# Kernel tuning notes

Hardware: AMD Instinct MI355X
Metric: run time of the kernel (lower is better)

## Reference

```python
import jax, jax.numpy as jnp
import numpy as np
import math

D_MODEL = 1024
N_HEADS = 16
D_HEAD = D_MODEL // N_HEADS
B, L = 4, 2048


def setup_inputs() -> dict:
    key = jax.random.key(0)
    ks = jax.random.split(key, 9)
    s = 1.0 / math.sqrt(D_MODEL)
    x = jax.random.normal(ks[0], (B, L, D_MODEL), dtype=jnp.float32)
    # causal mask, broadcastable over batch and heads
    attn_mask = jnp.tril(jnp.ones((L, L), dtype=jnp.int32))[None, None, :, :]
    Wq = jax.random.uniform(ks[1], (D_MODEL, D_MODEL), jnp.float32, -s, s)
    bq = jax.random.uniform(ks[2], (D_MODEL,), jnp.float32, -s, s)
    Wk = jax.random.uniform(ks[3], (D_MODEL, D_MODEL), jnp.float32, -s, s)
    bk = jax.random.uniform(ks[4], (D_MODEL,), jnp.float32, -s, s)
    Wv = jax.random.uniform(ks[5], (D_MODEL, D_MODEL), jnp.float32, -s, s)
    bv = jax.random.uniform(ks[6], (D_MODEL,), jnp.float32, -s, s)
    Wo = jax.random.uniform(ks[7], (D_MODEL, D_MODEL), jnp.float32, -s, s)
    bo = jax.random.uniform(ks[8], (D_MODEL,), jnp.float32, -s, s)
    return {"x": x, "attn_mask": attn_mask, "Wq": Wq, "bq": bq, "Wk": Wk,
            "bk": bk, "Wv": Wv, "bv": bv, "Wo": Wo, "bo": bo}


def reference(x, attn_mask, Wq, bq, Wk, bk, Wv, bv, Wo, bo):
    Bn, Ln, Dn = x.shape
    scale = 1.0 / math.sqrt(D_HEAD)

    def split_heads(t):  # [B,L,D] -> [B,H,L,dh]
        return t.reshape(Bn, Ln, N_HEADS, D_HEAD).transpose(0, 2, 1, 3)

    q = split_heads(x @ Wq + bq)
    k = split_heads(x @ Wk + bk)
    v = split_heads(x @ Wv + bv)
    scores = jnp.einsum('bhqd,bhkd->bhqk', q, k) * scale
    scores = jnp.where(attn_mask == 0, jnp.float32(-jnp.inf), scores)
    attn = jax.nn.softmax(scores, axis=-1)  # dropout p=0.0 -> identity
    ctx = jnp.einsum('bhqk,bhkd->bhqd', attn, v)
    ctx = ctx.transpose(0, 2, 1, 3).reshape(Bn, Ln, Dn)
    return ctx @ Wo + bo
```

## Files before the change

### kernel.cpp

```cpp
#include <hip/hip_runtime.h>


typedef unsigned short u16;
typedef __attribute__((ext_vector_type(8))) short short8;
typedef __attribute__((ext_vector_type(4))) float floatx4;
typedef __attribute__((ext_vector_type(2))) unsigned int uint2v;

#define NEG_BIG (-1e30f)
#define SCL_LOG2E 0.1803368801111244f

__device__ __forceinline__ u16 f2bf(float f) {
  unsigned int u = __builtin_bit_cast(unsigned int, f);
  u += 0x7fffu + ((u >> 16) & 1u);
  return (u16)(u >> 16);
}

__device__ __forceinline__ short8 cvt8(const float* __restrict__ p) {
  const floatx4 a = *(const floatx4*)p;
  const floatx4 b = *(const floatx4*)(p + 4);
  short8 r;
  r[0] = (short)f2bf(a[0]); r[1] = (short)f2bf(a[1]);
  r[2] = (short)f2bf(a[2]); r[3] = (short)f2bf(a[3]);
  r[4] = (short)f2bf(b[0]); r[5] = (short)f2bf(b[1]);
  r[6] = (short)f2bf(b[2]); r[7] = (short)f2bf(b[3]);
  return r;
}

__device__ __forceinline__ void gll16(const u16* g, u16* l) {
  __builtin_amdgcn_global_load_lds((const __attribute__((address_space(1))) void*)g,
                                   (__attribute__((address_space(3))) void*)l,
                                   16, 0, 0);
}

__global__ void cvt_x(const float* __restrict__ x, u16* __restrict__ xb) {
  const int i = blockIdx.x * 256 + threadIdx.x;
  *(short8*)(xb + (size_t)i * 8) = cvt8(x + (size_t)i * 8);
}

__global__ void transpose4(const float* __restrict__ s0, const float* __restrict__ s1,
                           const float* __restrict__ s2, const float* __restrict__ s3,
                           u16* __restrict__ d0, u16* __restrict__ d1,
                           u16* __restrict__ d2, u16* __restrict__ d3) {
  __shared__ u16 tile[64][72];
  const float* src; u16* dst;
  switch (blockIdx.z) {
    case 0: src = s0; dst = d0; break;
    case 1: src = s1; dst = d1; break;
    case 2: src = s2; dst = d2; break;
    default: src = s3; dst = d3; break;
  }
  const int t = threadIdx.x;
  const int c = t & 63, rg = t >> 6;
  const int x0 = blockIdx.x * 64, y0 = blockIdx.y * 64;
#pragma unroll
  for (int i = 0; i < 16; ++i) {
    const int row = rg * 16 + i;
    tile[row][c] = f2bf(src[(size_t)(y0 + row) * 1024 + x0 + c]);
  }
  __syncthreads();
#pragma unroll
  for (int i = 0; i < 16; ++i) {
    const int row = rg * 16 + i;
    dst[(size_t)(x0 + row) * 1024 + y0 + c] = tile[c][row];
  }
}

__global__ void transpose_v(const u16* __restrict__ Vb, u16* __restrict__ Vt) {
  __shared__ u16 tile[64][66];
  const int bh = blockIdx.y;
  const int l0 = blockIdx.x * 64;
  const size_t base = (size_t)bh * (2048 * 64);
  const int t = threadIdx.x;
#pragma unroll
  for (int c = t; c < 512; c += 256) {
    const int row = c >> 3, cc = c & 7;
    *(short8*)&tile[row][cc * 8] =
        *(const short8*)(Vb + base + (size_t)(l0 + row) * 64 + cc * 8);
  }
  __syncthreads();
  const int c2 = t & 63, rg = t >> 6;
#pragma unroll
  for (int i = 0; i < 16; ++i) {
    const int dr = rg * 16 + i;
    Vt[base + (size_t)dr * 2048 + l0 + c2] = tile[c2][dr];
  }
}

__global__ __launch_bounds__(256, 2) void gemm_qkv(
    const u16* __restrict__ A, const u16* __restrict__ Bt,
    const float* __restrict__ bq, const float* __restrict__ bk,
    const float* __restrict__ bv,
    u16* __restrict__ Qb, u16* __restrict__ Kb, u16* __restrict__ Vb) {
  const int K = 1024;
  __shared__ __align__(16) u16 As[128 * 32];
  __shared__ __align__(16) u16 Bs[128 * 32];
  const int t = threadIdx.x;
  const int w = t >> 6, l = t & 63;
  const int quad = l >> 4, l16 = l & 15;
  const int m0 = blockIdx.y * 128, n0 = blockIdx.x * 128;
  const int wr = w >> 1, wc = w & 1;

  floatx4 acc[4][4] = {};

  for (int k0 = 0; k0 < K; k0 += 32) {
    __syncthreads();
#pragma unroll
    for (int p = 0; p < 2; ++p) {
      const int c0 = (p * 4 + w) * 64;
      const int c = c0 + l;
      const int row = c >> 2;
      const int koff = (c & 3) * 8;
      gll16(A + (size_t)(m0 + row) * K + k0 + koff, &As[c0 * 8]);
      gll16(Bt + (size_t)(n0 + row) * K + k0 + koff, &Bs[c0 * 8]);
    }
    __syncthreads();

    short8 af[4], bf[4];
#pragma unroll
    for (int i = 0; i < 4; ++i)
      af[i] = *(const short8*)&As[(wr * 64 + i * 16 + l16) * 32 + quad * 8];
#pragma unroll
    for (int j = 0; j < 4; ++j)
      bf[j] = *(const short8*)&Bs[(wc * 64 + j * 16 + l16) * 32 + quad * 8];
#pragma unroll
    for (int i = 0; i < 4; ++i)
#pragma unroll
      for (int j = 0; j < 4; ++j)
        acc[i][j] = __builtin_amdgcn_mfma_f32_16x16x32_bf16(af[i], bf[j], acc[i][j], 0, 0, 0);
  }

  const int seg = n0 >> 10;
  const float* bias = (seg == 0) ? bq : (seg == 1) ? bk : bv;
  u16* dst = (seg == 0) ? Qb : (seg == 1) ? Kb : Vb;
#pragma unroll
  for (int j = 0; j < 4; ++j) {
    const int nn = (n0 & 1023) + wc * 64 + j * 16 + l16;
    const float bvs = bias[nn];
    const int h = nn >> 6, dh = nn & 63;
#pragma unroll
    for (int i = 0; i < 4; ++i) {
      const int rb = m0 + wr * 64 + i * 16 + quad * 4;
#pragma unroll
      for (int r = 0; r < 4; ++r) {
        const int m = rb + r;
        const int b = m >> 11, ll = m & 2047;
        dst[((size_t)(b * 16 + h) * 2048 + ll) * 64 + dh] = f2bf(acc[i][j][r] + bvs);
      }
    }
  }
}

__global__ __launch_bounds__(256, 2) void gemm_out(
    const u16* __restrict__ A, const u16* __restrict__ Bt,
    const float* __restrict__ bias, float* __restrict__ C, int M, int N, int K) {
  __shared__ __align__(16) u16 As[128 * 32];
  __shared__ __align__(16) u16 Bs[128 * 32];
  const int t = threadIdx.x;
  const int w = t >> 6, l = t & 63;
  const int quad = l >> 4, l16 = l & 15;
  const int m0 = blockIdx.y * 128, n0 = blockIdx.x * 128;
  const int wr = w >> 1, wc = w & 1;

  floatx4 acc[4][4] = {};

  for (int k0 = 0; k0 < K; k0 += 32) {
    __syncthreads();
#pragma unroll
    for (int p = 0; p < 2; ++p) {
      const int c0 = (p * 4 + w) * 64;
      const int c = c0 + l;
      const int row = c >> 2;
      const int koff = (c & 3) * 8;
      gll16(A + (size_t)(m0 + row) * K + k0 + koff, &As[c0 * 8]);
      gll16(Bt + (size_t)(n0 + row) * K + k0 + koff, &Bs[c0 * 8]);
    }
    __syncthreads();

    short8 af[4], bf[4];
#pragma unroll
    for (int i = 0; i < 4; ++i)
      af[i] = *(const short8*)&As[(wr * 64 + i * 16 + l16) * 32 + quad * 8];
#pragma unroll
    for (int j = 0; j < 4; ++j)
      bf[j] = *(const short8*)&Bs[(wc * 64 + j * 16 + l16) * 32 + quad * 8];
#pragma unroll
    for (int i = 0; i < 4; ++i)
#pragma unroll
      for (int j = 0; j < 4; ++j)
        acc[i][j] = __builtin_amdgcn_mfma_f32_16x16x32_bf16(af[i], bf[j], acc[i][j], 0, 0, 0);
  }

#pragma unroll
  for (int j = 0; j < 4; ++j) {
    const int n = n0 + wc * 64 + j * 16 + l16;
    const float bvs = bias[n];
#pragma unroll
    for (int i = 0; i < 4; ++i) {
      const int rb = m0 + wr * 64 + i * 16 + quad * 4;
#pragma unroll
      for (int r = 0; r < 4; ++r)
        C[(size_t)(rb + r) * N + n] = acc[i][j][r] + bvs;
    }
  }
}

__global__ __launch_bounds__(256, 4) void attn_kernel(
    const u16* __restrict__ Q, const u16* __restrict__ K,
    const u16* __restrict__ Vt, u16* __restrict__ ctx) {
  __shared__ __align__(16) u16 Ks[2][64 * 64];
  __shared__ __align__(16) u16 Vs[2][64 * 64];
  __shared__ __align__(16) u16 Ps[4 * 16 * 64];

  const int t = threadIdx.x;
  const int w = t >> 6, l = t & 63;
  const int quad = l >> 4, l16 = l & 15;
  const int bh = blockIdx.y;
  const size_t base = (size_t)bh * (2048 * 64);
  u16* Pw = &Ps[w * 16 * 64];
  unsigned int* Pw32 = (unsigned int*)Pw;
  const int b = bh >> 4, h = bh & 15;

  const int pc0 = w * 64 + l, pc1 = (4 + w) * 64 + l;
  const int sr0 = pc0 >> 3, sc0 = (pc0 & 7) ^ (sr0 & 7);
  const int sr1 = pc1 >> 3, sc1 = (pc1 & 7) ^ (sr1 & 7);
  const int swz = (l16 & 7);

  auto run_seg = [&](int q0, int nkt) {
    short8 aq[2];
#pragma unroll
    for (int ks = 0; ks < 2; ++ks)
      aq[ks] = *(const short8*)(Q + base + (size_t)(q0 + w * 16 + l16) * 64 + ks * 32 + quad * 8);

    gll16(K + base + (size_t)sr0 * 64 + sc0 * 8, &Ks[0][(w * 64) * 8]);
    gll16(K + base + (size_t)sr1 * 64 + sc1 * 8, &Ks[0][((4 + w) * 64) * 8]);
    gll16(Vt + base + (size_t)sr0 * 2048 + sc0 * 8, &Vs[0][(w * 64) * 8]);
    gll16(Vt + base + (size_t)sr1 * 2048 + sc1 * 8, &Vs[0][((4 + w) * 64) * 8]);

    floatx4 o[4] = {};
    float mrun = NEG_BIG, lsum = 0.f;

    auto body = [&](int kt, bool diag) {
      const int cur = kt & 1, nxt = cur ^ 1;
      __syncthreads();
      if (!diag) {
        const int kn = (kt + 1) * 64;
        gll16(K + base + (size_t)(kn + sr0) * 64 + sc0 * 8, &Ks[nxt][(w * 64) * 8]);
        gll16(K + base + (size_t)(kn + sr1) * 64 + sc1 * 8, &Ks[nxt][((4 + w) * 64) * 8]);
        gll16(Vt + base + (size_t)sr0 * 2048 + kn + sc0 * 8, &Vs[nxt][(w * 64) * 8]);
        gll16(Vt + base + (size_t)sr1 * 2048 + kn + sc1 * 8, &Vs[nxt][((4 + w) * 64) * 8]);
      }

      floatx4 s[4] = {};
#pragma unroll
      for (int ks = 0; ks < 2; ++ks)
#pragma unroll
        for (int tn = 0; tn < 4; ++tn) {
          const short8 bk = *(const short8*)&Ks[cur][(tn * 16 + l16) * 64 + (((ks * 4 + quad) ^ swz) << 3)];
          s[tn] = __builtin_amdgcn_mfma_f32_16x16x32_bf16(bk, aq[ks], s[tn], 0, 0, 0);
        }

      float mx = NEG_BIG;
#pragma unroll
      for (int tn = 0; tn < 4; ++tn)
#pragma unroll
        for (int r = 0; r < 4; ++r) {
          float v = s[tn][r] * SCL_LOG2E;
          if (diag && (tn * 16 + quad * 4 + r > w * 16 + l16)) v = NEG_BIG;
          s[tn][r] = v;
          mx = fmaxf(mx, v);
        }
      mx = fmaxf(mx, __shfl_xor(mx, 16));
      mx = fmaxf(mx, __shfl_xor(mx, 32));

      const float mnew = fmaxf(mrun, mx);
      const float alpha = exp2f(mrun - mnew);
      mrun = mnew;
      float rs = 0.f;
#pragma unroll
      for (int tn = 0; tn < 4; ++tn)
#pragma unroll
        for (int r = 0; r < 4; ++r) {
          const float p = exp2f(s[tn][r] - mnew);
          s[tn][r] = p;
          rs += p;
        }
      rs += __shfl_xor(rs, 16);
      rs += __shfl_xor(rs, 32);
      lsum = lsum * alpha + rs;
#pragma unroll
      for (int td = 0; td < 4; ++td)
#pragma unroll
        for (int r = 0; r < 4; ++r) o[td][r] *= alpha;

#pragma unroll
      for (int tn = 0; tn < 4; ++tn) {
        unsigned int p0, p1;
        asm("v_cvt_pk_bf16_f32 %0, %1, %2"
            : "=v"(p0) : "v"(s[tn][0]), "v"(s[tn][1]));
        asm("v_cvt_pk_bf16_f32 %0, %1, %2"
            : "=v"(p1) : "v"(s[tn][2]), "v"(s[tn][3]));
        const int cc = (2 * tn + (quad >> 1)) ^ swz;
        uint2v pr; pr.x = p0; pr.y = p1;
        *(uint2v*)&Pw32[l16 * 32 + cc * 4 + 2 * (quad & 1)] = pr;
      }
      __asm__ volatile("s_waitcnt lgkmcnt(0)" ::: "memory");
      __builtin_amdgcn_wave_barrier();

      short8 ap[2];
#pragma unroll
      for (int ks = 0; ks < 2; ++ks)
        ap[ks] = *(const short8*)&Pw[l16 * 64 + (((ks * 4 + quad) ^ swz) << 3)];

#pragma unroll
      for (int ks = 0; ks < 2; ++ks)
#pragma unroll
        for (int td = 0; td < 4; ++td) {
          const short8 bv = *(const short8*)&Vs[cur][(td * 16 + l16) * 64 + (((ks * 4 + quad) ^ swz) << 3)];
          o[td] = __builtin_amdgcn_mfma_f32_16x16x32_bf16(bv, ap[ks], o[td], 0, 0, 0);
        }
    };

    for (int kt = 0; kt < nkt - 1; ++kt) body(kt, false);
    body(nkt - 1, true);

    const float inv = 1.f / lsum;
    const int gq = q0 + w * 16 + l16;
    u16* crow = ctx + ((size_t)(b * 2048 + gq)) * 1024 + h * 64;
#pragma unroll
    for (int td = 0; td < 4; ++td) {
      unsigned int lo, hi;
      asm("v_cvt_pk_bf16_f32 %0, %1, %2"
          : "=v"(lo) : "v"(o[td][0] * inv), "v"(o[td][1] * inv));
      asm("v_cvt_pk_bf16_f32 %0, %1, %2"
          : "=v"(hi) : "v"(o[td][2] * inv), "v"(o[td][3] * inv));
      uint2v pk;
      pk.x = lo; pk.y = hi;
      *(uint2v*)(crow + td * 16 + quad * 4) = pk;
    }
  };

  const int bx = blockIdx.x;
  run_seg((31 - bx) * 64, 32 - bx);
  __syncthreads();
  run_seg(bx * 64, bx + 1);
}

extern "C" void kernel_launch(void* const* d_in, const int* in_sizes, int n_in,
                              void* d_out, int out_size, void* d_ws, size_t ws_size,
                              hipStream_t stream) {
  const float* x  = (const float*)d_in[0];
  const float* Wq = (const float*)d_in[2];
  const float* bq = (const float*)d_in[3];
  const float* Wk = (const float*)d_in[4];
  const float* bk = (const float*)d_in[5];
  const float* Wv = (const float*)d_in[6];
  const float* bv = (const float*)d_in[7];
  const float* Wo = (const float*)d_in[8];
  const float* bo = (const float*)d_in[9];

  u16* ws = (u16*)d_ws;
  const size_t WSZ = 1u << 20;
  const size_t TSZ = 8u << 20;
  u16* WqT = ws;
  u16* WkT = ws + WSZ;
  u16* WvT = ws + 2 * WSZ;
  u16* WoT = ws + 3 * WSZ;
  u16* xb  = ws + 4 * WSZ;
  u16* Qb  = xb + TSZ;
  u16* Kb  = Qb + TSZ;
  u16* Vb  = Kb + TSZ;
  u16* Vtb = xb;
  u16* Ctx = Vb;

  const dim3 tb(256);
  cvt_x<<<dim3(4096), tb, 0, stream>>>(x, xb);
  transpose4<<<dim3(16, 16, 4), tb, 0, stream>>>(Wq, Wk, Wv, Wo, WqT, WkT, WvT, WoT);
  gemm_qkv<<<dim3(24, 64), tb, 0, stream>>>(xb, WqT, bq, bk, bv, Qb, Kb, Vb);
  transpose_v<<<dim3(32, 64), tb, 0, stream>>>(Vb, Vtb);
  attn_kernel<<<dim3(16, 64), tb, 0, stream>>>(Qb, Kb, Vtb, Ctx);
  gemm_out<<<dim3(8, 64), tb, 0, stream>>>(Ctx, WoT, bo, (float*)d_out, 8192, 1024, 1024);
}
```

Baseline: 299.5 us.

## Rewrite attention with 32x32 MFMA, register-resident K/V and XCD-aware block mapping

The attention kernel now drops LDS staging for K/V and P. Each wave loads K and V fragments straight from global memory into registers, uses 32x32x16 MFMAs on 32-key tiles, and reshuffles P through cross-lane shuffles instead of LDS. The softmax scale is folded into Q in the QKV GEMM epilogue, and output rescaling is skipped when no row max rises. Blocks are remapped so each XCD handles a fixed set of heads, with per-wave causal work pairing and a halved grid. This removes LDS traffic and block barriers, but adds redundant global loads across waves and makes performance depend on L2 and cache locality.

```diff
diff --git a/kernel.cpp b/kernel.cpp
--- a/kernel.cpp
+++ b/kernel.cpp
@@ -4,7 +4,9 @@
 typedef unsigned short u16;
 typedef __attribute__((ext_vector_type(8))) short short8;
 typedef __attribute__((ext_vector_type(4))) float floatx4;
+typedef __attribute__((ext_vector_type(16))) float floatx16;
 typedef __attribute__((ext_vector_type(2))) unsigned int uint2v;
+typedef __attribute__((ext_vector_type(4))) unsigned int uint4v;
 
 #define NEG_BIG (-1e30f)
 #define SCL_LOG2E 0.1803368801111244f
@@ -132,6 +134,7 @@
   const int seg = n0 >> 10;
   const float* bias = (seg == 0) ? bq : (seg == 1) ? bk : bv;
   u16* dst = (seg == 0) ? Qb : (seg == 1) ? Kb : Vb;
+  const float scl = (seg == 0) ? SCL_LOG2E : 1.0f;
 #pragma unroll
   for (int j = 0; j < 4; ++j) {
     const int nn = (n0 & 1023) + wc * 64 + j * 16 + l16;
@@ -144,7 +147,7 @@
       for (int r = 0; r < 4; ++r) {
         const int m = rb + r;
         const int b = m >> 11, ll = m & 2047;
-        dst[((size_t)(b * 16 + h) * 2048 + ll) * 64 + dh] = f2bf(acc[i][j][r] + bvs);
+        dst[((size_t)(b * 16 + h) * 2048 + ll) * 64 + dh] = f2bf((acc[i][j][r] + bvs) * scl);
       }
     }
   }
@@ -204,145 +207,138 @@
   }
 }
 
-__global__ __launch_bounds__(256, 4) void attn_kernel(
+__global__ __launch_bounds__(256, 2) void attn_kernel(
     const u16* __restrict__ Q, const u16* __restrict__ K,
     const u16* __restrict__ Vt, u16* __restrict__ ctx) {
-  __shared__ __align__(16) u16 Ks[2][64 * 64];
-  __shared__ __align__(16) u16 Vs[2][64 * 64];
-  __shared__ __align__(16) u16 Ps[4 * 16 * 64];
-
   const int t = threadIdx.x;
   const int w = t >> 6, l = t & 63;
-  const int quad = l >> 4, l16 = l & 15;
-  const int bh = blockIdx.y;
+  const int l32 = l & 31, hi = l >> 5;
+
+  const int lin = blockIdx.y * 8 + blockIdx.x;
+  const int xcd = lin & 7, m = lin >> 3;
+  const int bh = xcd * 8 + (m & 7);
+  const int pairp = m >> 3;
   const size_t base = (size_t)bh * (2048 * 64);
-  u16* Pw = &Ps[w * 16 * 64];
-  unsigned int* Pw32 = (unsigned int*)Pw;
   const int b = bh >> 4, h = bh & 15;
 
-  const int pc0 = w * 64 + l, pc1 = (4 + w) * 64 + l;
-  const int sr0 = pc0 >> 3, sc0 = (pc0 & 7) ^ (sr0 & 7);
-  const int sr1 = pc1 >> 3, sc1 = (pc1 & 7) ^ (sr1 & 7);
-  const int swz = (l16 & 7);
-
-  auto run_seg = [&](int q0, int nkt) {
-    short8 aq[2];
-#pragma unroll
-    for (int ks = 0; ks < 2; ++ks)
-      aq[ks] = *(const short8*)(Q + base + (size_t)(q0 + w * 16 + l16) * 64 + ks * 32 + quad * 8);
-
-    gll16(K + base + (size_t)sr0 * 64 + sc0 * 8, &Ks[0][(w * 64) * 8]);
-    gll16(K + base + (size_t)sr1 * 64 + sc1 * 8, &Ks[0][((4 + w) * 64) * 8]);
-    gll16(Vt + base + (size_t)sr0 * 2048 + sc0 * 8, &Vs[0][(w * 64) * 8]);
-    gll16(Vt + base + (size_t)sr1 * 2048 + sc1 * 8, &Vs[0][((4 + w) * 64) * 8]);
-
-    floatx4 o[4] = {};
+  auto seg = [&](int qblk, int qw) {
+    const int qsub = qblk * 128 + qw * 32;
+    const int nkt = qblk * 4 + qw + 1;
+    const int qg = qsub + l32;
+
+    short8 qf[4];
+#pragma unroll
+    for (int ks = 0; ks < 4; ++ks)
+      qf[ks] = *(const short8*)(Q + base + (size_t)qg * 64 + ks * 16 + hi * 8);
+    short8 kf[4];
+#pragma unroll
+    for (int ks = 0; ks < 4; ++ks)
+      kf[ks] = *(const short8*)(K + base + (size_t)l32 * 64 + ks * 16 + hi * 8);
+
+    floatx16 o0 = {}, o1 = {};
     float mrun = NEG_BIG, lsum = 0.f;
 
     auto body = [&](int kt, bool diag) {
-      const int cur = kt & 1, nxt = cur ^ 1;
-      __syncthreads();
+      short8 vf[4];
+#pragma unroll
+      for (int dw = 0; dw < 2; ++dw)
+#pragma unroll
+        for (int k2 = 0; k2 < 2; ++k2)
+          vf[dw * 2 + k2] = *(const short8*)(Vt + base + (size_t)(dw * 32 + l32) * 2048 +
+                                             kt * 32 + k2 * 16 + hi * 8);
+
+      floatx16 sA = {};
+#pragma unroll
+      for (int ks = 0; ks < 4; ++ks)
+        sA = __builtin_amdgcn_mfma_f32_32x32x16_bf16(kf[ks], qf[ks], sA, 0, 0, 0);
+
       if (!diag) {
-        const int kn = (kt + 1) * 64;
-        gll16(K + base + (size_t)(kn + sr0) * 64 + sc0 * 8, &Ks[nxt][(w * 64) * 8]);
-        gll16(K + base + (size_t)(kn + sr1) * 64 + sc1 * 8, &Ks[nxt][((4 + w) * 64) * 8]);
-        gll16(Vt + base + (size_t)sr0 * 2048 + kn + sc0 * 8, &Vs[nxt][(w * 64) * 8]);
-        gll16(Vt + base + (size_t)sr1 * 2048 + kn + sc1 * 8, &Vs[nxt][((4 + w) * 64) * 8]);
-      }
-
-      floatx4 s[4] = {};
-#pragma unroll
-      for (int ks = 0; ks < 2; ++ks)
-#pragma unroll
-        for (int tn = 0; tn < 4; ++tn) {
-          const short8 bk = *(const short8*)&Ks[cur][(tn * 16 + l16) * 64 + (((ks * 4 + quad) ^ swz) << 3)];
-          s[tn] = __builtin_amdgcn_mfma_f32_16x16x32_bf16(bk, aq[ks], s[tn], 0, 0, 0);
-        }
+#pragma unroll
+        for (int ks = 0; ks < 4; ++ks)
+          kf[ks] = *(const short8*)(K + base + (size_t)((kt + 1) * 32 + l32) * 64 +
+                                    ks * 16 + hi * 8);
+      }
 
       float mx = NEG_BIG;
-#pragma unroll
-      for (int tn = 0; tn < 4; ++tn)
-#pragma unroll
-        for (int r = 0; r < 4; ++r) {
-          float v = s[tn][r] * SCL_LOG2E;
-          if (diag && (tn * 16 + quad * 4 + r > w * 16 + l16)) v = NEG_BIG;
-          s[tn][r] = v;
+      if (diag) {
+#pragma unroll
+        for (int r = 0; r < 16; ++r) {
+          const int krow = (r & 3) + 8 * (r >> 2) + 4 * hi;
+          float v = sA[r];
+          if (krow > l32) v = NEG_BIG;
+          sA[r] = v;
           mx = fmaxf(mx, v);
         }
-      mx = fmaxf(mx, __shfl_xor(mx, 16));
+      } else {
+#pragma unroll
+        for (int r = 0; r < 16; ++r) mx = fmaxf(mx, sA[r]);
+      }
       mx = fmaxf(mx, __shfl_xor(mx, 32));
 
-      const float mnew = fmaxf(mrun, mx);
-      const float alpha = exp2f(mrun - mnew);
-      mrun = mnew;
+      if (__any(mx > mrun)) {
+        const float mnew = fmaxf(mrun, mx);
+        const float al = exp2f(mrun - mnew);
+        mrun = mnew;
+        lsum *= al;
+#pragma unroll
+        for (int r = 0; r < 16; ++r) { o0[r] *= al; o1[r] *= al; }
+      }
+
       float rs = 0.f;
 #pragma unroll
-      for (int tn = 0; tn < 4; ++tn)
-#pragma unroll
-        for (int r = 0; r < 4; ++r) {
-          const float p = exp2f(s[tn][r] - mnew);
-          s[tn][r] = p;
-          rs += p;
-        }
-      rs += __shfl_xor(rs, 16);
+      for (int r = 0; r < 16; ++r) {
+        const float p = exp2f(sA[r] - mrun);
+        sA[r] = p;
+        rs += p;
+      }
       rs += __shfl_xor(rs, 32);
-      lsum = lsum * alpha + rs;
-#pragma unroll
-      for (int td = 0; td < 4; ++td)
-#pragma unroll
-        for (int r = 0; r < 4; ++r) o[td][r] *= alpha;
-
-#pragma unroll
-      for (int tn = 0; tn < 4; ++tn) {
-        unsigned int p0, p1;
+      lsum += rs;
+
+      unsigned int wv[8], xv[8];
+#pragma unroll
+      for (int i = 0; i < 8; ++i)
         asm("v_cvt_pk_bf16_f32 %0, %1, %2"
-            : "=v"(p0) : "v"(s[tn][0]), "v"(s[tn][1]));
-        asm("v_cvt_pk_bf16_f32 %0, %1, %2"
-            : "=v"(p1) : "v"(s[tn][2]), "v"(s[tn][3]));
-        const int cc = (2 * tn + (quad >> 1)) ^ swz;
-        uint2v pr; pr.x = p0; pr.y = p1;
-        *(uint2v*)&Pw32[l16 * 32 + cc * 4 + 2 * (quad & 1)] = pr;
-      }
-      __asm__ volatile("s_waitcnt lgkmcnt(0)" ::: "memory");
-      __builtin_amdgcn_wave_barrier();
-
-      short8 ap[2];
-#pragma unroll
-      for (int ks = 0; ks < 2; ++ks)
-        ap[ks] = *(const short8*)&Pw[l16 * 64 + (((ks * 4 + quad) ^ swz) << 3)];
-
-#pragma unroll
-      for (int ks = 0; ks < 2; ++ks)
-#pragma unroll
-        for (int td = 0; td < 4; ++td) {
-          const short8 bv = *(const short8*)&Vs[cur][(td * 16 + l16) * 64 + (((ks * 4 + quad) ^ swz) << 3)];
-          o[td] = __builtin_amdgcn_mfma_f32_16x16x32_bf16(bv, ap[ks], o[td], 0, 0, 0);
-        }
+            : "=v"(wv[i]) : "v"(sA[2 * i]), "v"(sA[2 * i + 1]));
+#pragma unroll
+      for (int i = 0; i < 8; ++i) xv[i] = __shfl_xor(wv[i], 32);
+      uint4v f0, f1;
+      f0[0] = hi ? xv[2] : wv[0];  f0[1] = hi ? xv[3] : wv[1];
+      f0[2] = hi ? wv[2] : xv[0];  f0[3] = hi ? wv[3] : xv[1];
+      f1[0] = hi ? xv[6] : wv[4];  f1[1] = hi ? xv[7] : wv[5];
+      f1[2] = hi ? wv[6] : xv[4];  f1[3] = hi ? wv[7] : xv[5];
+      const short8 ap0 = __builtin_bit_cast(short8, f0);
+      const short8 ap1 = __builtin_bit_cast(short8, f1);
+
+      o0 = __builtin_amdgcn_mfma_f32_32x32x16_bf16(vf[0], ap0, o0, 0, 0, 0);
+      o0 = __builtin_amdgcn_mfma_f32_32x32x16_bf16(vf[1], ap1, o0, 0, 0, 0);
+      o1 = __builtin_amdgcn_mfma_f32_32x32x16_bf16(vf[2], ap0, o1, 0, 0, 0);
+      o1 = __builtin_amdgcn_mfma_f32_32x32x16_bf16(vf[3], ap1, o1, 0, 0, 0);
     };
 
-    for (int kt = 0; kt < nkt - 1; ++kt) body(kt, false);
+    for (int kt = 0; kt + 1 < nkt; ++kt) body(kt, false);
     body(nkt - 1, true);
 
     const float inv = 1.f / lsum;
-    const int gq = q0 + w * 16 + l16;
-    u16* crow = ctx + ((size_t)(b * 2048 + gq)) * 1024 + h * 64;
-#pragma unroll
-    for (int td = 0; td < 4; ++td) {
-      unsigned int lo, hi;
-      asm("v_cvt_pk_bf16_f32 %0, %1, %2"
-          : "=v"(lo) : "v"(o[td][0] * inv), "v"(o[td][1] * inv));
-      asm("v_cvt_pk_bf16_f32 %0, %1, %2"
-          : "=v"(hi) : "v"(o[td][2] * inv), "v"(o[td][3] * inv));
-      uint2v pk;
-      pk.x = lo; pk.y = hi;
-      *(uint2v*)(crow + td * 16 + quad * 4) = pk;
+    u16* crow = ctx + ((size_t)(b * 2048 + qg)) * 1024 + h * 64;
+#pragma unroll
+    for (int dw = 0; dw < 2; ++dw) {
+#pragma unroll
+      for (int run = 0; run < 4; ++run) {
+        const float a0 = (dw ? o1[run * 4 + 0] : o0[run * 4 + 0]) * inv;
+        const float a1 = (dw ? o1[run * 4 + 1] : o0[run * 4 + 1]) * inv;
+        const float a2 = (dw ? o1[run * 4 + 2] : o0[run * 4 + 2]) * inv;
+        const float a3 = (dw ? o1[run * 4 + 3] : o0[run * 4 + 3]) * inv;
+        unsigned int lo, hw;
+        asm("v_cvt_pk_bf16_f32 %0, %1, %2" : "=v"(lo) : "v"(a0), "v"(a1));
+        asm("v_cvt_pk_bf16_f32 %0, %1, %2" : "=v"(hw) : "v"(a2), "v"(a3));
+        uint2v pk; pk.x = lo; pk.y = hw;
+        *(uint2v*)(crow + dw * 32 + run * 8 + hi * 4) = pk;
+      }
     }
   };
 
-  const int bx = blockIdx.x;
-  run_seg((31 - bx) * 64, 32 - bx);
-  __syncthreads();
-  run_seg(bx * 64, bx + 1);
+  seg(15 - pairp, w);
+  seg(pairp, 3 - w);
 }
 
 extern "C" void kernel_launch(void* const* d_in, const int* in_sizes, int n_in,
@@ -377,6 +373,6 @@
   transpose4<<<dim3(16, 16, 4), tb, 0, stream>>>(Wq, Wk, Wv, Wo, WqT, WkT, WvT, WoT);
   gemm_qkv<<<dim3(24, 64), tb, 0, stream>>>(xb, WqT, bq, bk, bv, Qb, Kb, Vb);
   transpose_v<<<dim3(32, 64), tb, 0, stream>>>(Vb, Vtb);
-  attn_kernel<<<dim3(16, 64), tb, 0, stream>>>(Qb, Kb, Vtb, Ctx);
+  attn_kernel<<<dim3(8, 64), tb, 0, stream>>>(Qb, Kb, Vtb, Ctx);
   gemm_out<<<dim3(8, 64), tb, 0, stream>>>(Ctx, WoT, bo, (float*)d_out, 8192, 1024, 1024);
 }
```

Result: slower. 338.2 us (+12.9%).

## Enlarge attention blocks to 8 waves with lazy rescale and folded Q scaling

Applied to the files above, without the earlier changes.

Attention blocks grow to 512 threads and cover 128 query rows per segment, so each K/V tile loaded into shared memory serves twice as many queries. Block-to-(batch,head) mapping is reordered, and the softmax scale times log2e is folded into the Q projection epilogue. The kernel skips fully masked tiles per wave, masks only diagonal tiles, and rescales the running max only when it grows by more than 8. It also adds s_setprio around the MFMA sections. The costs are waves idling on skipped tiles while the block still syncs, and Q being stored pre-scaled in bf16.

```diff
diff --git a/kernel.cpp b/kernel.cpp
--- a/kernel.cpp
+++ b/kernel.cpp
@@ -132,6 +132,7 @@
   const int seg = n0 >> 10;
   const float* bias = (seg == 0) ? bq : (seg == 1) ? bk : bv;
   u16* dst = (seg == 0) ? Qb : (seg == 1) ? Kb : Vb;
+  const float scl = (seg == 0) ? SCL_LOG2E : 1.0f;
 #pragma unroll
   for (int j = 0; j < 4; ++j) {
     const int nn = (n0 & 1023) + wc * 64 + j * 16 + l16;
@@ -144,7 +145,7 @@
       for (int r = 0; r < 4; ++r) {
         const int m = rb + r;
         const int b = m >> 11, ll = m & 2047;
-        dst[((size_t)(b * 16 + h) * 2048 + ll) * 64 + dh] = f2bf(acc[i][j][r] + bvs);
+        dst[((size_t)(b * 16 + h) * 2048 + ll) * 64 + dh] = f2bf((acc[i][j][r] + bvs) * scl);
       }
     }
   }
@@ -204,53 +205,60 @@
   }
 }
 
-__global__ __launch_bounds__(256, 4) void attn_kernel(
+__global__ __launch_bounds__(512, 4) void attn_kernel(
     const u16* __restrict__ Q, const u16* __restrict__ K,
     const u16* __restrict__ Vt, u16* __restrict__ ctx) {
   __shared__ __align__(16) u16 Ks[2][64 * 64];
   __shared__ __align__(16) u16 Vs[2][64 * 64];
-  __shared__ __align__(16) u16 Ps[4 * 16 * 64];
+  __shared__ __align__(16) u16 Ps[8 * 16 * 64];
 
   const int t = threadIdx.x;
   const int w = t >> 6, l = t & 63;
   const int quad = l >> 4, l16 = l & 15;
-  const int bh = blockIdx.y;
+  const int lin = blockIdx.y * 8 + blockIdx.x;
+  const int bh = (lin & 7) * 8 + ((lin >> 3) & 7);
+  const int pp = lin >> 6;
   const size_t base = (size_t)bh * (2048 * 64);
+  const int b = bh >> 4, h = bh & 15;
   u16* Pw = &Ps[w * 16 * 64];
   unsigned int* Pw32 = (unsigned int*)Pw;
-  const int b = bh >> 4, h = bh & 15;
-
-  const int pc0 = w * 64 + l, pc1 = (4 + w) * 64 + l;
-  const int sr0 = pc0 >> 3, sc0 = (pc0 & 7) ^ (sr0 & 7);
-  const int sr1 = pc1 >> 3, sc1 = (pc1 & 7) ^ (sr1 & 7);
+
+  const int pc = w * 64 + l;
+  const int sr = pc >> 3, sc = (pc & 7) ^ (sr & 7);
   const int swz = (l16 & 7);
 
-  auto run_seg = [&](int q0, int nkt) {
+  auto run_seg = [&](int p) {
+    const int q0 = p * 128;
+    const int nkt = 2 * p + 2;
+    const int qg = q0 + w * 16 + l16;
+    const int qmax = q0 + w * 16 + 15;
+    const int qmin = q0 + w * 16;
+
     short8 aq[2];
 #pragma unroll
     for (int ks = 0; ks < 2; ++ks)
-      aq[ks] = *(const short8*)(Q + base + (size_t)(q0 + w * 16 + l16) * 64 + ks * 32 + quad * 8);
-
-    gll16(K + base + (size_t)sr0 * 64 + sc0 * 8, &Ks[0][(w * 64) * 8]);
-    gll16(K + base + (size_t)sr1 * 64 + sc1 * 8, &Ks[0][((4 + w) * 64) * 8]);
-    gll16(Vt + base + (size_t)sr0 * 2048 + sc0 * 8, &Vs[0][(w * 64) * 8]);
-    gll16(Vt + base + (size_t)sr1 * 2048 + sc1 * 8, &Vs[0][((4 + w) * 64) * 8]);
+      aq[ks] = *(const short8*)(Q + base + (size_t)qg * 64 + ks * 32 + quad * 8);
+
+    gll16(K + base + (size_t)sr * 64 + sc * 8, &Ks[0][(w * 64) * 8]);
+    gll16(Vt + base + (size_t)sr * 2048 + sc * 8, &Vs[0][(w * 64) * 8]);
 
     floatx4 o[4] = {};
     float mrun = NEG_BIG, lsum = 0.f;
 
-    auto body = [&](int kt, bool diag) {
+    for (int kt = 0; kt < nkt; ++kt) {
       const int cur = kt & 1, nxt = cur ^ 1;
       __syncthreads();
-      if (!diag) {
+      if (kt + 1 < nkt) {
         const int kn = (kt + 1) * 64;
-        gll16(K + base + (size_t)(kn + sr0) * 64 + sc0 * 8, &Ks[nxt][(w * 64) * 8]);
-        gll16(K + base + (size_t)(kn + sr1) * 64 + sc1 * 8, &Ks[nxt][((4 + w) * 64) * 8]);
-        gll16(Vt + base + (size_t)sr0 * 2048 + kn + sc0 * 8, &Vs[nxt][(w * 64) * 8]);
-        gll16(Vt + base + (size_t)sr1 * 2048 + kn + sc1 * 8, &Vs[nxt][((4 + w) * 64) * 8]);
-      }
+        gll16(K + base + (size_t)(kn + sr) * 64 + sc * 8, &Ks[nxt][(w * 64) * 8]);
+        gll16(Vt + base + (size_t)sr * 2048 + kn + sc * 8, &Vs[nxt][(w * 64) * 8]);
+      }
+      const int kbase = kt * 64;
+      if (kbase > qmax) continue;
+      const bool masked = (kbase + 63 > qmin);
 
       floatx4 s[4] = {};
+      __builtin_amdgcn_s_setprio(1);
 #pragma unroll
       for (int ks = 0; ks < 2; ++ks)
 #pragma unroll
@@ -258,39 +266,48 @@
           const short8 bk = *(const short8*)&Ks[cur][(tn * 16 + l16) * 64 + (((ks * 4 + quad) ^ swz) << 3)];
           s[tn] = __builtin_amdgcn_mfma_f32_16x16x32_bf16(bk, aq[ks], s[tn], 0, 0, 0);
         }
+      __builtin_amdgcn_s_setprio(0);
 
       float mx = NEG_BIG;
-#pragma unroll
-      for (int tn = 0; tn < 4; ++tn)
-#pragma unroll
-        for (int r = 0; r < 4; ++r) {
-          float v = s[tn][r] * SCL_LOG2E;
-          if (diag && (tn * 16 + quad * 4 + r > w * 16 + l16)) v = NEG_BIG;
-          s[tn][r] = v;
-          mx = fmaxf(mx, v);
-        }
+      if (masked) {
+#pragma unroll
+        for (int tn = 0; tn < 4; ++tn)
+#pragma unroll
+          for (int r = 0; r < 4; ++r) {
+            float v = s[tn][r];
+            if (kbase + tn * 16 + quad * 4 + r > qg) v = NEG_BIG;
+            s[tn][r] = v;
+            mx = fmaxf(mx, v);
+          }
+      } else {
+#pragma unroll
+        for (int tn = 0; tn < 4; ++tn)
+#pragma unroll
+          for (int r = 0; r < 4; ++r) mx = fmaxf(mx, s[tn][r]);
+      }
       mx = fmaxf(mx, __shfl_xor(mx, 16));
       mx = fmaxf(mx, __shfl_xor(mx, 32));
 
-      const float mnew = fmaxf(mrun, mx);
-      const float alpha = exp2f(mrun - mnew);
-      mrun = mnew;
+      if (!__all(mx - mrun <= 8.f)) {
+        const float mnew = fmaxf(mrun, mx);
+        const float al = exp2f(mrun - mnew);
+        mrun = mnew;
+        lsum *= al;
+#pragma unroll
+        for (int td = 0; td < 4; ++td)
+#pragma unroll
+          for (int r = 0; r < 4; ++r) o[td][r] *= al;
+      }
+
       float rs = 0.f;
 #pragma unroll
       for (int tn = 0; tn < 4; ++tn)
 #pragma unroll
         for (int r = 0; r < 4; ++r) {
-          const float p = exp2f(s[tn][r] - mnew);
-          s[tn][r] = p;
-          rs += p;
+          const float pv = exp2f(s[tn][r] - mrun);
+          s[tn][r] = pv;
+          rs += pv;
         }
-      rs += __shfl_xor(rs, 16);
-      rs += __shfl_xor(rs, 32);
-      lsum = lsum * alpha + rs;
-#pragma unroll
-      for (int td = 0; td < 4; ++td)
-#pragma unroll
-        for (int r = 0; r < 4; ++r) o[td][r] *= alpha;
 
 #pragma unroll
       for (int tn = 0; tn < 4; ++tn) {
@@ -303,6 +320,9 @@
         uint2v pr; pr.x = p0; pr.y = p1;
         *(uint2v*)&Pw32[l16 * 32 + cc * 4 + 2 * (quad & 1)] = pr;
       }
+      rs += __shfl_xor(rs, 16);
+      rs += __shfl_xor(rs, 32);
+      lsum += rs;
       __asm__ volatile("s_waitcnt lgkmcnt(0)" ::: "memory");
       __builtin_amdgcn_wave_barrier();
 
@@ -311,6 +331,7 @@
       for (int ks = 0; ks < 2; ++ks)
         ap[ks] = *(const short8*)&Pw[l16 * 64 + (((ks * 4 + quad) ^ swz) << 3)];
 
+      __builtin_amdgcn_s_setprio(1);
 #pragma unroll
       for (int ks = 0; ks < 2; ++ks)
 #pragma unroll
@@ -318,14 +339,11 @@
           const short8 bv = *(const short8*)&Vs[cur][(td * 16 + l16) * 64 + (((ks * 4 + quad) ^ swz) << 3)];
           o[td] = __builtin_amdgcn_mfma_f32_16x16x32_bf16(bv, ap[ks], o[td], 0, 0, 0);
         }
-    };
-
-    for (int kt = 0; kt < nkt - 1; ++kt) body(kt, false);
-    body(nkt - 1, true);
+      __builtin_amdgcn_s_setprio(0);
+    }
 
     const float inv = 1.f / lsum;
-    const int gq = q0 + w * 16 + l16;
-    u16* crow = ctx + ((size_t)(b * 2048 + gq)) * 1024 + h * 64;
+    u16* crow = ctx + ((size_t)(b * 2048 + qg)) * 1024 + h * 64;
 #pragma unroll
     for (int td = 0; td < 4; ++td) {
       unsigned int lo, hi;
@@ -339,10 +357,9 @@
     }
   };
 
-  const int bx = blockIdx.x;
-  run_seg((31 - bx) * 64, 32 - bx);
+  run_seg(15 - pp);
   __syncthreads();
-  run_seg(bx * 64, bx + 1);
+  run_seg(pp);
 }
 
 extern "C" void kernel_launch(void* const* d_in, const int* in_sizes, int n_in,
@@ -377,6 +394,6 @@
   transpose4<<<dim3(16, 16, 4), tb, 0, stream>>>(Wq, Wk, Wv, Wo, WqT, WkT, WvT, WoT);
   gemm_qkv<<<dim3(24, 64), tb, 0, stream>>>(xb, WqT, bq, bk, bv, Qb, Kb, Vb);
   transpose_v<<<dim3(32, 64), tb, 0, stream>>>(Vb, Vtb);
-  attn_kernel<<<dim3(16, 64), tb, 0, stream>>>(Qb, Kb, Vtb, Ctx);
+  attn_kernel<<<dim3(8, 64), dim3(512), 0, stream>>>(Qb, Kb, Vtb, Ctx);
   gemm_out<<<dim3(8, 64), tb, 0, stream>>>(Ctx, WoT, bo, (float*)d_out, 8192, 1024, 1024);
 }
```

Result: faster. 292.3 us (-2.4%).
